# Kernel tuning notes

Measured on AMD Instinct MI355X. Metric: run time of the kernel, lower is better.

Reference implementation:

```python
import jax, jax.numpy as jnp
import numpy as np

B = 64           # batch size
N = 512          # number of nodes
E = 1            # edge feature dims of the GSO
M = 256          # nodes carrying edge-variant weights (hybrid EV since M < N)
F = [1, 8, 8]    # node-signal features per layer
K = [3, 3]       # shift taps per layer
MLP = [512, 128] # readout dims
P_EDGE = 0.03    # graph density
ZTOL = 1e-9      # zero tolerance for sparsity pattern


def setup_inputs():
    ks = jax.random.split(jax.random.key(0), 13)
    x = jax.random.normal(ks[0], (B, F[0], N), dtype=jnp.float32)
    adj = (jax.random.uniform(ks[1], (E, N, N)) < P_EDGE).astype(jnp.float32)
    S = adj * jax.random.normal(ks[2], (E, N, N), dtype=jnp.float32) / np.sqrt(N * P_EDGE)

    def w(k, shape, scale):
        return jax.random.normal(k, shape, dtype=jnp.float32) * np.float32(scale)

    wEV1 = w(ks[3], (F[1], E, K[0], F[0], N, N), 1.0 / np.sqrt(F[0] * N))
    wLSI1 = w(ks[4], (F[1], E, K[0], F[0]), 1.0 / np.sqrt(F[0] * K[0]))
    b1 = w(ks[5], (F[1], 1), 0.1)
    wEV2 = w(ks[6], (F[2], E, K[1], F[1], N, N), 1.0 / np.sqrt(F[1] * N))
    wLSI2 = w(ks[7], (F[2], E, K[1], F[1]), 1.0 / np.sqrt(F[1] * K[1]))
    b2 = w(ks[8], (F[2], 1), 0.1)
    W1 = w(ks[9], (MLP[0], F[2] * N), 1.0 / np.sqrt(F[2] * N))
    bW1 = w(ks[10], (MLP[0],), 0.1)
    W2 = w(ks[11], (MLP[1], MLP[0]), 1.0 / np.sqrt(MLP[0]))
    bW2 = w(ks[12], (MLP[1],), 0.1)
    return dict(x=x, S=S, wEV1=wEV1, wLSI1=wLSI1, b1=b1,
                wEV2=wEV2, wLSI2=wLSI2, b2=b2, W1=W1, bW1=bW1, W2=W2, bW2=bW2)


def _sparsity_mask(S):
    # support of S + I, then kill the [M:, M:] block (hybrid EV mask)
    eye = jnp.eye(N, dtype=S.dtype)
    sp = ((jnp.abs(S) + eye[None]) > ZTOL).astype(S.dtype)      # (E,N,N)
    hyb = jnp.ones((N, N), S.dtype).at[M:, M:].set(0.0)
    return sp * hyb[None]


def _ev_layer(xl, S, sp, wEV, wLSI, b):
    # xl: (B,G,N); wEV: (F,E,K,G,N,N); wLSI: (F,E,K,G); b: (F,1)
    Phi = wEV * sp[None, :, None, None]                          # masked filter matrices
    Kl = wEV.shape[2]
    # EV part: y = sum_k Phi^(k) ... Phi^(0) x, summed over e, g
    z = jnp.einsum('fegmn,bgn->bfegm', Phi[:, :, 0], xl)
    y = z
    for k in range(1, Kl):
        z = jnp.einsum('fegmn,bfegn->bfegm', Phi[:, :, k], z)
        y = y + z
    y = y.sum(axis=(2, 3))                                       # (B,F,N)
    # LSI part of the hybrid filter: sum_{e,k,g} h_{fekg} S_e^k x_g
    xe = jnp.broadcast_to(xl[:, None], (xl.shape[0], S.shape[0]) + xl.shape[1:])
    zs = [xe]                                                    # k = 0: identity
    for k in range(1, Kl):
        zs.append(jnp.einsum('emn,begn->begm', S, zs[-1]))
    zst = jnp.stack(zs, axis=2)                                  # (B,E,K,G,N)
    y = y + jnp.einsum('fekg,bekgn->bfn', wLSI, zst)
    return y + b[None]                                           # bias broadcast over nodes


def reference(x, S, wEV1, wLSI1, b1, wEV2, wLSI2, b2, W1, bW1, W2, bW2):
    sp = _sparsity_mask(S)
    # order=None -> permIdentity, so x[:, :, order] == x; NoPool is identity
    y = _ev_layer(x, S, sp, wEV1, wLSI1, b1)
    y = _ev_layer(y, S, sp, wEV2, wLSI2, b2)
    yf = y.reshape(y.shape[0], -1)                               # (B, F[-1]*N)
    h = yf @ W1.T + bW1                                          # linear MLP (no activation)
    return h @ W2.T + bW2
```

## Files before the change

kernel.cpp:

```cpp
#include <hip/hip_runtime.h>
#include <cstdint>
#include <cstddef>

#define NNODE 512
#define MMASK 256
#define ZT 1e-9f
#define NPL 216

__global__ __launch_bounds__(256) void k_prep(const float* __restrict__ x,
                                              const float* __restrict__ S,
                                              int* __restrict__ sp_col, int* __restrict__ sp_cnt,
                                              int* __restrict__ s_col, float* __restrict__ s_val,
                                              int* __restrict__ s_cnt,
                                              float* __restrict__ xt) {
  int gtid = blockIdx.x * 256 + threadIdx.x;
  int W = gtid >> 6, lane = threadIdx.x & 63;
  {
    int n = gtid >> 6, b = gtid & 63;
    xt[gtid] = x[b * NNODE + n];
  }
  int m = W;
  int csp = 0, cs = 0;
  unsigned long long lt = (1ull << lane) - 1ull;
  for (int ch = 0; ch < 8; ++ch) {
    int n = ch * 64 + lane;
    float s = S[m * NNODE + n];
    bool ps  = (s != 0.f);
    bool psp = ((fabsf(s) + ((m == n) ? 1.f : 0.f)) > ZT) && !((m >= MMASK) && (n >= MMASK));
    unsigned long long msp = __ballot(psp), ms = __ballot(ps);
    if (psp) { int p = csp + __popcll(msp & lt); if (p < 64) sp_col[(m << 6) + p] = n; }
    if (ps)  { int p = cs  + __popcll(ms  & lt); if (p < 64) { s_col[(m << 6) + p] = n; s_val[(m << 6) + p] = s; } }
    csp += __popcll(msp); cs += __popcll(ms);
  }
  if (lane >= csp) sp_col[(m << 6) + lane] = 0;
  if (lane >= cs)  { s_col[(m << 6) + lane] = 0; s_val[(m << 6) + lane] = 0.f; }
  if (lane == 0) { sp_cnt[m] = (csp < 64 ? csp : 64); s_cnt[m] = (cs < 64 ? cs : 64); }
}

__global__ __launch_bounds__(256) void k_pack(const float* __restrict__ wEV1,
                                              const float* __restrict__ wEV2,
                                              const int* __restrict__ sp_col,
                                              const int* __restrict__ sp_cnt,
                                              float* __restrict__ wpk) {
  __shared__ float rowbuf[4][512];
  int wv = threadIdx.x >> 6, lane = threadIdx.x & 63;
  int W = blockIdx.x * 4 + wv;
  int nwv = gridDim.x * 4;
  for (int job = W; job < NPL * NNODE; job += nwv) {
    int p = job >> 9, r = job & 511;
    const float* src = ((p < 24) ? (wEV1 + ((size_t)p << 18))
                                 : (wEV2 + ((size_t)(p - 24) << 18))) + (r << 9);
    float4 a = ((const float4*)src)[lane];
    float4 b = ((const float4*)src)[64 + lane];
    ((float4*)rowbuf[wv])[lane] = a;
    ((float4*)rowbuf[wv])[64 + lane] = b;
    int cl = sp_col[(r << 6) + lane];
    float wl = (lane < sp_cnt[r]) ? rowbuf[wv][cl] : 0.f;
    wpk[((size_t)p << 15) + (r << 6) + lane] = wl;
  }
}

__device__ __forceinline__ float ell_mac(int cl, float wl, int cnt,
                                         const float* __restrict__ zin, int lane) {
  float acc = 0.f;
  for (int base = 0; base < cnt; base += 16) {
    float z[16];
#pragma unroll
    for (int i = 0; i < 16; ++i) {
      int c = __shfl(cl, base + i);
      z[i] = zin[(c << 6) + lane];
    }
#pragma unroll
    for (int i = 0; i < 16; ++i) acc += __shfl(wl, base + i) * z[i];
  }
  return acc;
}

__global__ __launch_bounds__(256) void k_l1s0(const float* __restrict__ wpk,
    const int* __restrict__ sp_col, const int* __restrict__ sp_cnt,
    const int* __restrict__ s_col, const float* __restrict__ s_val, const int* __restrict__ s_cnt,
    const float* __restrict__ xt, float* __restrict__ zA1, float* __restrict__ u1) {
  int W = (blockIdx.x * 256 + threadIdx.x) >> 6, lane = threadIdx.x & 63;
  int nwv = (gridDim.x << 2);
  for (int u = W; u < 4608; u += nwv) {
    if (u < 4096) {
      int f = u >> 9, r = u & 511;
      float wl = wpk[((size_t)(f * 3 + 0) << 15) + (r << 6) + lane];
      int cl = sp_col[(r << 6) + lane];
      zA1[((size_t)f << 15) + (r << 6) + lane] = ell_mac(cl, wl, sp_cnt[r], xt, lane);
    } else {
      int r = u - 4096;
      int cl = s_col[(r << 6) + lane];
      float wl = s_val[(r << 6) + lane];
      u1[(r << 6) + lane] = ell_mac(cl, wl, s_cnt[r], xt, lane);
    }
  }
}

__global__ __launch_bounds__(256) void k_l1s1(const float* __restrict__ wpk,
    const int* __restrict__ sp_col, const int* __restrict__ sp_cnt,
    const int* __restrict__ s_col, const float* __restrict__ s_val, const int* __restrict__ s_cnt,
    const float* __restrict__ zA1, const float* __restrict__ u1,
    float* __restrict__ zB1, float* __restrict__ u2) {
  int W = (blockIdx.x * 256 + threadIdx.x) >> 6, lane = threadIdx.x & 63;
  int nwv = (gridDim.x << 2);
  for (int u = W; u < 4608; u += nwv) {
    if (u < 4096) {
      int f = u >> 9, r = u & 511;
      float wl = wpk[((size_t)(f * 3 + 1) << 15) + (r << 6) + lane];
      int cl = sp_col[(r << 6) + lane];
      zB1[((size_t)f << 15) + (r << 6) + lane] =
          ell_mac(cl, wl, sp_cnt[r], zA1 + ((size_t)f << 15), lane);
    } else {
      int r = u - 4096;
      int cl = s_col[(r << 6) + lane];
      float wl = s_val[(r << 6) + lane];
      u2[(r << 6) + lane] = ell_mac(cl, wl, s_cnt[r], u1, lane);
    }
  }
}

__global__ __launch_bounds__(256) void k_l1s2(const float* __restrict__ wpk,
    const int* __restrict__ sp_col, const int* __restrict__ sp_cnt,
    const float* __restrict__ zA1, const float* __restrict__ zB1,
    const float* __restrict__ xt, const float* __restrict__ u1, const float* __restrict__ u2,
    const float* __restrict__ wLSI1, const float* __restrict__ b1, float* __restrict__ y1) {
  int W = (blockIdx.x * 256 + threadIdx.x) >> 6, lane = threadIdx.x & 63;
  int nwv = (gridDim.x << 2);
  for (int u = W; u < 4096; u += nwv) {
    int f = u >> 9, r = u & 511;
    float wl = wpk[((size_t)(f * 3 + 2) << 15) + (r << 6) + lane];
    int cl = sp_col[(r << 6) + lane];
    float a = ell_mac(cl, wl, sp_cnt[r], zB1 + ((size_t)f << 15), lane);
    int idx = (r << 6) + lane;
    size_t fi = ((size_t)f << 15) + idx;
    y1[fi] = zA1[fi] + zB1[fi] + a
           + wLSI1[f * 3 + 0] * xt[idx] + wLSI1[f * 3 + 1] * u1[idx]
           + wLSI1[f * 3 + 2] * u2[idx] + b1[f];
  }
}

__global__ __launch_bounds__(256) void k_l2s0(const float* __restrict__ wpk,
    const int* __restrict__ sp_col, const int* __restrict__ sp_cnt,
    const int* __restrict__ s_col, const float* __restrict__ s_val, const int* __restrict__ s_cnt,
    const float* __restrict__ y1, float* __restrict__ zA2, float* __restrict__ v1) {
  int W = (blockIdx.x * 256 + threadIdx.x) >> 6, lane = threadIdx.x & 63;
  int nwv = (gridDim.x << 2);
  for (int u = W; u < 36864; u += nwv) {
    if (u < 32768) {
      int c = u >> 9, r = u & 511;
      int f = c >> 3, g = c & 7;
      float wl = wpk[((size_t)(24 + (f * 3 + 0) * 8 + g) << 15) + (r << 6) + lane];
      int cl = sp_col[(r << 6) + lane];
      zA2[((size_t)c << 15) + (r << 6) + lane] =
          ell_mac(cl, wl, sp_cnt[r], y1 + ((size_t)g << 15), lane);
    } else {
      int t = u - 32768;
      int g = t >> 9, r = t & 511;
      int cl = s_col[(r << 6) + lane];
      float wl = s_val[(r << 6) + lane];
      v1[((size_t)g << 15) + (r << 6) + lane] =
          ell_mac(cl, wl, s_cnt[r], y1 + ((size_t)g << 15), lane);
    }
  }
}

__global__ __launch_bounds__(256) void k_l2s1(const float* __restrict__ wpk,
    const int* __restrict__ sp_col, const int* __restrict__ sp_cnt,
    const int* __restrict__ s_col, const float* __restrict__ s_val, const int* __restrict__ s_cnt,
    const float* __restrict__ zA2, const float* __restrict__ v1,
    float* __restrict__ zB2, float* __restrict__ v2) {
  int W = (blockIdx.x * 256 + threadIdx.x) >> 6, lane = threadIdx.x & 63;
  int nwv = (gridDim.x << 2);
  for (int u = W; u < 36864; u += nwv) {
    if (u < 32768) {
      int c = u >> 9, r = u & 511;
      int f = c >> 3, g = c & 7;
      float wl = wpk[((size_t)(24 + (f * 3 + 1) * 8 + g) << 15) + (r << 6) + lane];
      int cl = sp_col[(r << 6) + lane];
      zB2[((size_t)c << 15) + (r << 6) + lane] =
          ell_mac(cl, wl, sp_cnt[r], zA2 + ((size_t)c << 15), lane);
    } else {
      int t = u - 32768;
      int g = t >> 9, r = t & 511;
      int cl = s_col[(r << 6) + lane];
      float wl = s_val[(r << 6) + lane];
      v2[((size_t)g << 15) + (r << 6) + lane] =
          ell_mac(cl, wl, s_cnt[r], v1 + ((size_t)g << 15), lane);
    }
  }
}

__global__ __launch_bounds__(256) void k_l2s2(const float* __restrict__ wpk,
    const int* __restrict__ sp_col, const int* __restrict__ sp_cnt,
    const float* __restrict__ zA2, const float* __restrict__ zB2,
    const float* __restrict__ y1, const float* __restrict__ v1, const float* __restrict__ v2,
    const float* __restrict__ wLSI2, const float* __restrict__ b2,
    const float* __restrict__ bW1, float* __restrict__ y2, float* __restrict__ ht) {
  int gtid = blockIdx.x * 256 + threadIdx.x;
  int W = gtid >> 6, lane = threadIdx.x & 63;
  int nwv = (gridDim.x << 2);
  if (gtid < 32768) ht[gtid] = bW1[gtid >> 6];
  for (int u = W; u < 4096; u += nwv) {
    int f = u >> 9, r = u & 511;
    int idx = (r << 6) + lane;
    int cl = sp_col[(r << 6) + lane];
    int cnt = sp_cnt[r];
    float acc = b2[f];
#pragma unroll
    for (int g = 0; g < 8; ++g) {
      int c = f * 8 + g;
      float wl = wpk[((size_t)(24 + (f * 3 + 2) * 8 + g) << 15) + (r << 6) + lane];
      float a = ell_mac(cl, wl, cnt, zB2 + ((size_t)c << 15), lane);
      size_t ci = ((size_t)c << 15) + idx;
      size_t gi = ((size_t)g << 15) + idx;
      acc += zA2[ci] + zB2[ci] + a
           + wLSI2[f * 24 + g]      * y1[gi]
           + wLSI2[f * 24 + 8 + g]  * v1[gi]
           + wLSI2[f * 24 + 16 + g] * v2[gi];
    }
    y2[((size_t)f << 15) + idx] = acc;
  }
}

__global__ __launch_bounds__(256) void k_gemm1(const float* __restrict__ W1,
                                               const float* __restrict__ y2,
                                               const float* __restrict__ bW2,
                                               float* __restrict__ ht,
                                               float* __restrict__ out) {
  int gtid = blockIdx.x * 256 + threadIdx.x;
  int W = gtid >> 6, lane = threadIdx.x & 63;
  int nwv = (gridDim.x << 2);
  if (gtid < 8192) out[gtid] = bW2[gtid & 127];
  for (int u = W; u < 2048; u += nwv) {
    int pg = u >> 5, qs = u & 31;
    const float* wrow = W1 + (size_t)pg * 8 * 4096 + qs * 128;
    const float* yb = y2 + ((size_t)(qs * 128) << 6);
    float acc[8] = {0, 0, 0, 0, 0, 0, 0, 0};
    for (int q = 0; q < 128; q += 8) {
      float yv[8];
#pragma unroll
      for (int i = 0; i < 8; ++i) yv[i] = yb[((q + i) << 6) + lane];
#pragma unroll
      for (int i = 0; i < 8; ++i) {
#pragma unroll
        for (int p = 0; p < 8; ++p) acc[p] += wrow[(size_t)p * 4096 + q + i] * yv[i];
      }
    }
#pragma unroll
    for (int p = 0; p < 8; ++p) atomicAdd(&ht[((pg * 8 + p) << 6) + lane], acc[p]);
  }
}

__global__ __launch_bounds__(256) void k_gemm2(const float* __restrict__ W2,
                                               const float* __restrict__ ht,
                                               float* __restrict__ out) {
  int W = (blockIdx.x * 256 + threadIdx.x) >> 6, lane = threadIdx.x & 63;
  int nwv = (gridDim.x << 2);
  for (int u = W; u < 1024; u += nwv) {
    int o = u >> 3, qs = u & 7;
    const float* w2 = W2 + (size_t)o * 512 + qs * 64;
    const float* hb = ht + ((size_t)(qs * 64) << 6);
    float acc = 0.f;
    for (int q = 0; q < 64; q += 8) {
#pragma unroll
      for (int i = 0; i < 8; ++i) acc += w2[q + i] * hb[((q + i) << 6) + lane];
    }
    atomicAdd(&out[lane * 128 + o], acc);
  }
}

extern "C" void kernel_launch(void* const* d_in, const int* in_sizes, int n_in,
                              void* d_out, int out_size, void* d_ws, size_t ws_size,
                              hipStream_t stream) {
  const float* x     = (const float*)d_in[0];
  const float* S     = (const float*)d_in[1];
  const float* wEV1  = (const float*)d_in[2];
  const float* wLSI1 = (const float*)d_in[3];
  const float* b1    = (const float*)d_in[4];
  const float* wEV2  = (const float*)d_in[5];
  const float* wLSI2 = (const float*)d_in[6];
  const float* b2    = (const float*)d_in[7];
  const float* W1    = (const float*)d_in[8];
  const float* bW1   = (const float*)d_in[9];
  const float* W2    = (const float*)d_in[10];
  const float* bW2   = (const float*)d_in[11];
  float* out = (float*)d_out;

  char* w = (char*)d_ws;
  auto alloc = [&](size_t bytes) { char* p = w; w += (bytes + 255) & ~(size_t)255; return p; };
  int*   sp_col = (int*)alloc(512 * 64 * 4);
  int*   sp_cnt = (int*)alloc(512 * 4);
  int*   s_col  = (int*)alloc(512 * 64 * 4);
  float* s_val  = (float*)alloc(512 * 64 * 4);
  int*   s_cnt  = (int*)alloc(512 * 4);
  float* wpk    = (float*)alloc((size_t)NPL * 32768 * 4);
  float* xt     = (float*)alloc((size_t)32768 * 4);
  float* u1     = (float*)alloc((size_t)32768 * 4);
  float* u2     = (float*)alloc((size_t)32768 * 4);
  float* zA1    = (float*)alloc((size_t)8 * 32768 * 4);
  float* zB1    = (float*)alloc((size_t)8 * 32768 * 4);
  float* y1     = (float*)alloc((size_t)8 * 32768 * 4);
  float* zA2    = (float*)alloc((size_t)64 * 32768 * 4);
  float* zB2    = (float*)alloc((size_t)64 * 32768 * 4);
  float* v1     = (float*)alloc((size_t)8 * 32768 * 4);
  float* v2     = (float*)alloc((size_t)8 * 32768 * 4);
  float* y2     = (float*)alloc((size_t)8 * 32768 * 4);
  float* ht     = (float*)alloc((size_t)32768 * 4);
  (void)ws_size; (void)in_sizes; (void)n_in; (void)out_size;

  k_prep<<<128, 256, 0, stream>>>(x, S, sp_col, sp_cnt, s_col, s_val, s_cnt, xt);
  k_pack<<<1024, 256, 0, stream>>>(wEV1, wEV2, sp_col, sp_cnt, wpk);
  k_l1s0<<<256, 256, 0, stream>>>(wpk, sp_col, sp_cnt, s_col, s_val, s_cnt, xt, zA1, u1);
  k_l1s1<<<256, 256, 0, stream>>>(wpk, sp_col, sp_cnt, s_col, s_val, s_cnt, zA1, u1, zB1, u2);
  k_l1s2<<<256, 256, 0, stream>>>(wpk, sp_col, sp_cnt, zA1, zB1, xt, u1, u2, wLSI1, b1, y1);
  k_l2s0<<<1024, 256, 0, stream>>>(wpk, sp_col, sp_cnt, s_col, s_val, s_cnt, y1, zA2, v1);
  k_l2s1<<<1024, 256, 0, stream>>>(wpk, sp_col, sp_cnt, s_col, s_val, s_cnt, zA2, v1, zB2, v2);
  k_l2s2<<<512, 256, 0, stream>>>(wpk, sp_col, sp_cnt, zA2, zB2, y1, v1, v2, wLSI2, b2, bW1, y2, ht);
  k_gemm1<<<128, 256, 0, stream>>>(W1, y2, bW2, ht, out);
  k_gemm2<<<64, 256, 0, stream>>>(W2, ht, out);
}
```

Before: 495.3 us.

## Use scalar loads for ELL columns and weights, and launch one wave per row

```diff
diff --git a/kernel.cpp b/kernel.cpp
--- a/kernel.cpp
+++ b/kernel.cpp
@@ -44,7 +44,7 @@
                                               float* __restrict__ wpk) {
   __shared__ float rowbuf[4][512];
   int wv = threadIdx.x >> 6, lane = threadIdx.x & 63;
-  int W = blockIdx.x * 4 + wv;
+  int W = __builtin_amdgcn_readfirstlane(blockIdx.x * 4 + wv);
   int nwv = gridDim.x * 4;
   for (int job = W; job < NPL * NNODE; job += nwv) {
     int p = job >> 9, r = job & 511;
@@ -60,39 +60,44 @@
   }
 }
 
-__device__ __forceinline__ float ell_mac(int cl, float wl, int cnt,
-                                         const float* __restrict__ zin, int lane) {
-  float acc = 0.f;
+__device__ __forceinline__ float ell_mac_s(const int* __restrict__ cols,
+                                           const float* __restrict__ ws,
+                                           int cnt,
+                                           const float* __restrict__ zin, int lane) {
+  float a0 = 0.f, a1 = 0.f, a2 = 0.f, a3 = 0.f;
   for (int base = 0; base < cnt; base += 16) {
-    float z[16];
-#pragma unroll
-    for (int i = 0; i < 16; ++i) {
-      int c = __shfl(cl, base + i);
-      z[i] = zin[(c << 6) + lane];
-    }
-#pragma unroll
-    for (int i = 0; i < 16; ++i) acc += __shfl(wl, base + i) * z[i];
-  }
-  return acc;
+#pragma unroll
+    for (int i = 0; i < 16; i += 4) {
+      int   c0 = cols[base + i    ]; float w0 = ws[base + i    ];
+      int   c1 = cols[base + i + 1]; float w1 = ws[base + i + 1];
+      int   c2 = cols[base + i + 2]; float w2 = ws[base + i + 2];
+      int   c3 = cols[base + i + 3]; float w3 = ws[base + i + 3];
+      a0 += w0 * zin[(c0 << 6) + lane];
+      a1 += w1 * zin[(c1 << 6) + lane];
+      a2 += w2 * zin[(c2 << 6) + lane];
+      a3 += w3 * zin[(c3 << 6) + lane];
+    }
+  }
+  return (a0 + a1) + (a2 + a3);
 }
 
 __global__ __launch_bounds__(256) void k_l1s0(const float* __restrict__ wpk,
     const int* __restrict__ sp_col, const int* __restrict__ sp_cnt,
     const int* __restrict__ s_col, const float* __restrict__ s_val, const int* __restrict__ s_cnt,
     const float* __restrict__ xt, float* __restrict__ zA1, float* __restrict__ u1) {
-  int W = (blockIdx.x * 256 + threadIdx.x) >> 6, lane = threadIdx.x & 63;
+  int lane = threadIdx.x & 63;
+  int W = __builtin_amdgcn_readfirstlane((blockIdx.x * 256 + (int)threadIdx.x) >> 6);
   int nwv = (gridDim.x << 2);
   for (int u = W; u < 4608; u += nwv) {
     if (u < 4096) {
       int f = u >> 9, r = u & 511;
-      float wl = wpk[((size_t)(f * 3 + 0) << 15) + (r << 6) + lane];
-      int cl = sp_col[(r << 6) + lane];
-      zA1[((size_t)f << 15) + (r << 6) + lane] = ell_mac(cl, wl, sp_cnt[r], xt, lane);
+      zA1[((size_t)f << 15) + (r << 6) + lane] =
+          ell_mac_s(sp_col + (r << 6), wpk + ((size_t)(f * 3 + 0) << 15) + (r << 6),
+                    sp_cnt[r], xt, lane);
     } else {
       int r = u - 4096;
-      int cl = s_col[(r << 6) + lane];
-      float wl = s_val[(r << 6) + lane];
-      u1[(r << 6) + lane] = ell_mac(cl, wl, s_cnt[r], xt, lane);
+      u1[(r << 6) + lane] =
+          ell_mac_s(s_col + (r << 6), s_val + (r << 6), s_cnt[r], xt, lane);
     }
   }
 }
@@ -102,20 +107,19 @@
     const int* __restrict__ s_col, const float* __restrict__ s_val, const int* __restrict__ s_cnt,
     const float* __restrict__ zA1, const float* __restrict__ u1,
     float* __restrict__ zB1, float* __restrict__ u2) {
-  int W = (blockIdx.x * 256 + threadIdx.x) >> 6, lane = threadIdx.x & 63;
+  int lane = threadIdx.x & 63;
+  int W = __builtin_amdgcn_readfirstlane((blockIdx.x * 256 + (int)threadIdx.x) >> 6);
   int nwv = (gridDim.x << 2);
   for (int u = W; u < 4608; u += nwv) {
     if (u < 4096) {
       int f = u >> 9, r = u & 511;
-      float wl = wpk[((size_t)(f * 3 + 1) << 15) + (r << 6) + lane];
-      int cl = sp_col[(r << 6) + lane];
       zB1[((size_t)f << 15) + (r << 6) + lane] =
-          ell_mac(cl, wl, sp_cnt[r], zA1 + ((size_t)f << 15), lane);
+          ell_mac_s(sp_col + (r << 6), wpk + ((size_t)(f * 3 + 1) << 15) + (r << 6),
+                    sp_cnt[r], zA1 + ((size_t)f << 15), lane);
     } else {
       int r = u - 4096;
-      int cl = s_col[(r << 6) + lane];
-      float wl = s_val[(r << 6) + lane];
-      u2[(r << 6) + lane] = ell_mac(cl, wl, s_cnt[r], u1, lane);
+      u2[(r << 6) + lane] =
+          ell_mac_s(s_col + (r << 6), s_val + (r << 6), s_cnt[r], u1, lane);
     }
   }
 }
@@ -125,13 +129,13 @@
     const float* __restrict__ zA1, const float* __restrict__ zB1,
     const float* __restrict__ xt, const float* __restrict__ u1, const float* __restrict__ u2,
     const float* __restrict__ wLSI1, const float* __restrict__ b1, float* __restrict__ y1) {
-  int W = (blockIdx.x * 256 + threadIdx.x) >> 6, lane = threadIdx.x & 63;
+  int lane = threadIdx.x & 63;
+  int W = __builtin_amdgcn_readfirstlane((blockIdx.x * 256 + (int)threadIdx.x) >> 6);
   int nwv = (gridDim.x << 2);
   for (int u = W; u < 4096; u += nwv) {
     int f = u >> 9, r = u & 511;
-    float wl = wpk[((size_t)(f * 3 + 2) << 15) + (r << 6) + lane];
-    int cl = sp_col[(r << 6) + lane];
-    float a = ell_mac(cl, wl, sp_cnt[r], zB1 + ((size_t)f << 15), lane);
+    float a = ell_mac_s(sp_col + (r << 6), wpk + ((size_t)(f * 3 + 2) << 15) + (r << 6),
+                        sp_cnt[r], zB1 + ((size_t)f << 15), lane);
     int idx = (r << 6) + lane;
     size_t fi = ((size_t)f << 15) + idx;
     y1[fi] = zA1[fi] + zB1[fi] + a
@@ -144,23 +148,23 @@
     const int* __restrict__ sp_col, const int* __restrict__ sp_cnt,
     const int* __restrict__ s_col, const float* __restrict__ s_val, const int* __restrict__ s_cnt,
     const float* __restrict__ y1, float* __restrict__ zA2, float* __restrict__ v1) {
-  int W = (blockIdx.x * 256 + threadIdx.x) >> 6, lane = threadIdx.x & 63;
+  int lane = threadIdx.x & 63;
+  int W = __builtin_amdgcn_readfirstlane((blockIdx.x * 256 + (int)threadIdx.x) >> 6);
   int nwv = (gridDim.x << 2);
   for (int u = W; u < 36864; u += nwv) {
     if (u < 32768) {
       int c = u >> 9, r = u & 511;
       int f = c >> 3, g = c & 7;
-      float wl = wpk[((size_t)(24 + (f * 3 + 0) * 8 + g) << 15) + (r << 6) + lane];
-      int cl = sp_col[(r << 6) + lane];
       zA2[((size_t)c << 15) + (r << 6) + lane] =
-          ell_mac(cl, wl, sp_cnt[r], y1 + ((size_t)g << 15), lane);
+          ell_mac_s(sp_col + (r << 6),
+                    wpk + ((size_t)(24 + (f * 3 + 0) * 8 + g) << 15) + (r << 6),
+                    sp_cnt[r], y1 + ((size_t)g << 15), lane);
     } else {
       int t = u - 32768;
       int g = t >> 9, r = t & 511;
-      int cl = s_col[(r << 6) + lane];
-      float wl = s_val[(r << 6) + lane];
       v1[((size_t)g << 15) + (r << 6) + lane] =
-          ell_mac(cl, wl, s_cnt[r], y1 + ((size_t)g << 15), lane);
+          ell_mac_s(s_col + (r << 6), s_val + (r << 6), s_cnt[r],
+                    y1 + ((size_t)g << 15), lane);
     }
   }
 }
@@ -170,23 +174,23 @@
     const int* __restrict__ s_col, const float* __restrict__ s_val, const int* __restrict__ s_cnt,
     const float* __restrict__ zA2, const float* __restrict__ v1,
     float* __restrict__ zB2, float* __restrict__ v2) {
-  int W = (blockIdx.x * 256 + threadIdx.x) >> 6, lane = threadIdx.x & 63;
+  int lane = threadIdx.x & 63;
+  int W = __builtin_amdgcn_readfirstlane((blockIdx.x * 256 + (int)threadIdx.x) >> 6);
   int nwv = (gridDim.x << 2);
   for (int u = W; u < 36864; u += nwv) {
     if (u < 32768) {
       int c = u >> 9, r = u & 511;
       int f = c >> 3, g = c & 7;
-      float wl = wpk[((size_t)(24 + (f * 3 + 1) * 8 + g) << 15) + (r << 6) + lane];
-      int cl = sp_col[(r << 6) + lane];
       zB2[((size_t)c << 15) + (r << 6) + lane] =
-          ell_mac(cl, wl, sp_cnt[r], zA2 + ((size_t)c << 15), lane);
+          ell_mac_s(sp_col + (r << 6),
+                    wpk + ((size_t)(24 + (f * 3 + 1) * 8 + g) << 15) + (r << 6),
+                    sp_cnt[r], zA2 + ((size_t)c << 15), lane);
     } else {
       int t = u - 32768;
       int g = t >> 9, r = t & 511;
-      int cl = s_col[(r << 6) + lane];
-      float wl = s_val[(r << 6) + lane];
       v2[((size_t)g << 15) + (r << 6) + lane] =
-          ell_mac(cl, wl, s_cnt[r], v1 + ((size_t)g << 15), lane);
+          ell_mac_s(s_col + (r << 6), s_val + (r << 6), s_cnt[r],
+                    v1 + ((size_t)g << 15), lane);
     }
   }
 }
@@ -198,20 +202,22 @@
     const float* __restrict__ wLSI2, const float* __restrict__ b2,
     const float* __restrict__ bW1, float* __restrict__ y2, float* __restrict__ ht) {
   int gtid = blockIdx.x * 256 + threadIdx.x;
-  int W = gtid >> 6, lane = threadIdx.x & 63;
+  int lane = threadIdx.x & 63;
+  int W = __builtin_amdgcn_readfirstlane(gtid >> 6);
   int nwv = (gridDim.x << 2);
   if (gtid < 32768) ht[gtid] = bW1[gtid >> 6];
   for (int u = W; u < 4096; u += nwv) {
     int f = u >> 9, r = u & 511;
     int idx = (r << 6) + lane;
-    int cl = sp_col[(r << 6) + lane];
+    const int* cols = sp_col + (r << 6);
     int cnt = sp_cnt[r];
     float acc = b2[f];
 #pragma unroll
     for (int g = 0; g < 8; ++g) {
       int c = f * 8 + g;
-      float wl = wpk[((size_t)(24 + (f * 3 + 2) * 8 + g) << 15) + (r << 6) + lane];
-      float a = ell_mac(cl, wl, cnt, zB2 + ((size_t)c << 15), lane);
+      float a = ell_mac_s(cols,
+                          wpk + ((size_t)(24 + (f * 3 + 2) * 8 + g) << 15) + (r << 6),
+                          cnt, zB2 + ((size_t)c << 15), lane);
       size_t ci = ((size_t)c << 15) + idx;
       size_t gi = ((size_t)g << 15) + idx;
       acc += zA2[ci] + zB2[ci] + a
@@ -229,7 +235,8 @@
                                                float* __restrict__ ht,
                                                float* __restrict__ out) {
   int gtid = blockIdx.x * 256 + threadIdx.x;
-  int W = gtid >> 6, lane = threadIdx.x & 63;
+  int lane = threadIdx.x & 63;
+  int W = __builtin_amdgcn_readfirstlane(gtid >> 6);
   int nwv = (gridDim.x << 2);
   if (gtid < 8192) out[gtid] = bW2[gtid & 127];
   for (int u = W; u < 2048; u += nwv) {
@@ -255,7 +262,8 @@
 __global__ __launch_bounds__(256) void k_gemm2(const float* __restrict__ W2,
                                                const float* __restrict__ ht,
                                                float* __restrict__ out) {
-  int W = (blockIdx.x * 256 + threadIdx.x) >> 6, lane = threadIdx.x & 63;
+  int lane = threadIdx.x & 63;
+  int W = __builtin_amdgcn_readfirstlane((blockIdx.x * 256 + (int)threadIdx.x) >> 6);
   int nwv = (gridDim.x << 2);
   for (int u = W; u < 1024; u += nwv) {
     int o = u >> 3, qs = u & 7;
@@ -310,13 +318,13 @@
   (void)ws_size; (void)in_sizes; (void)n_in; (void)out_size;
 
   k_prep<<<128, 256, 0, stream>>>(x, S, sp_col, sp_cnt, s_col, s_val, s_cnt, xt);
-  k_pack<<<1024, 256, 0, stream>>>(wEV1, wEV2, sp_col, sp_cnt, wpk);
-  k_l1s0<<<256, 256, 0, stream>>>(wpk, sp_col, sp_cnt, s_col, s_val, s_cnt, xt, zA1, u1);
-  k_l1s1<<<256, 256, 0, stream>>>(wpk, sp_col, sp_cnt, s_col, s_val, s_cnt, zA1, u1, zB1, u2);
-  k_l1s2<<<256, 256, 0, stream>>>(wpk, sp_col, sp_cnt, zA1, zB1, xt, u1, u2, wLSI1, b1, y1);
-  k_l2s0<<<1024, 256, 0, stream>>>(wpk, sp_col, sp_cnt, s_col, s_val, s_cnt, y1, zA2, v1);
-  k_l2s1<<<1024, 256, 0, stream>>>(wpk, sp_col, sp_cnt, s_col, s_val, s_cnt, zA2, v1, zB2, v2);
-  k_l2s2<<<512, 256, 0, stream>>>(wpk, sp_col, sp_cnt, zA2, zB2, y1, v1, v2, wLSI2, b2, bW1, y2, ht);
-  k_gemm1<<<128, 256, 0, stream>>>(W1, y2, bW2, ht, out);
-  k_gemm2<<<64, 256, 0, stream>>>(W2, ht, out);
-}
+  k_pack<<<2048, 256, 0, stream>>>(wEV1, wEV2, sp_col, sp_cnt, wpk);
+  k_l1s0<<<1152, 256, 0, stream>>>(wpk, sp_col, sp_cnt, s_col, s_val, s_cnt, xt, zA1, u1);
+  k_l1s1<<<1152, 256, 0, stream>>>(wpk, sp_col, sp_cnt, s_col, s_val, s_cnt, zA1, u1, zB1, u2);
+  k_l1s2<<<1024, 256, 0, stream>>>(wpk, sp_col, sp_cnt, zA1, zB1, xt, u1, u2, wLSI1, b1, y1);
+  k_l2s0<<<9216, 256, 0, stream>>>(wpk, sp_col, sp_cnt, s_col, s_val, s_cnt, y1, zA2, v1);
+  k_l2s1<<<9216, 256, 0, stream>>>(wpk, sp_col, sp_cnt, s_col, s_val, s_cnt, zA2, v1, zB2, v2);
+  k_l2s2<<<1024, 256, 0, stream>>>(wpk, sp_col, sp_cnt, zA2, zB2, y1, v1, v2, wLSI2, b2, bW1, y2, ht);
+  k_gemm1<<<512, 256, 0, stream>>>(W1, y2, bW2, ht, out);
+  k_gemm2<<<256, 256, 0, stream>>>(W2, ht, out);
+}
```

Result: faster. 409.9 us (-17.3%).
